# Performance work log

Measured on AMD Instinct MI355X. Metric: run time of the kernel, lower is better.

## Reference

```python
import jax, jax.numpy as jnp
import numpy as np
from jax import lax

B, S, E, CC, H, NH, K = 8, 2048, 128, 256, 256, 8, 7
HD = H // NH  # head dim = 32


def setup_inputs() -> dict:
    key = jax.random.key(0)
    ks = jax.random.split(key, 16)
    x = jax.random.normal(ks[0], (B, S, E), dtype=jnp.float32)
    lengths = jax.random.randint(ks[1], (B,), S // 2, S + 1)
    mask = (jnp.arange(S)[None, :] < lengths[:, None])  # contiguous prefix padding mask
    sc = 0.02
    return {
        "x": x,
        "mask": mask,
        "conv_w": jax.random.normal(ks[2], (CC, E, K), dtype=jnp.float32) * sc,
        "conv_b": jnp.zeros((CC,), jnp.float32),
        "wq": jax.random.normal(ks[3], (CC, H), dtype=jnp.float32) * sc,
        "bq": jnp.zeros((H,), jnp.float32),
        "wk": jax.random.normal(ks[4], (CC, H), dtype=jnp.float32) * sc,
        "bk": jnp.zeros((H,), jnp.float32),
        "wv": jax.random.normal(ks[5], (CC, H), dtype=jnp.float32) * sc,
        "bv": jnp.zeros((H,), jnp.float32),
        "fc_w": jax.random.normal(ks[6], (H, CC), dtype=jnp.float32) * sc,
        "fc_b": jnp.zeros((CC,), jnp.float32),
        "ln_g": jnp.ones((CC,), jnp.float32),
        "ln_b": jnp.zeros((CC,), jnp.float32),
        "gamma": jnp.float32(0.5),
        "std_param": jnp.float32(0.2),
    }


def _penalty(mask, gamma, std_param):
    # (B, S, S) Gaussian penalty, nonzero only in the valid_len x valid_len block
    valid_len = mask.sum(axis=-1).astype(jnp.float32)  # (B,)
    idx = jnp.arange(S, dtype=jnp.float32)
    valid = (jnp.arange(S)[None, :] < mask.sum(axis=-1)[:, None]).astype(jnp.float32)  # (B,S)
    norm_pos = (idx[None, :] + 1.0) / (valid_len[:, None] + 1.0)  # (B,S)
    std = jnp.clip(std_param, 0.01, 0.5)
    base = jnp.exp(-((norm_pos - 0.5) ** 2) / (2.0 * std * std))
    pvec = base * (jnp.exp(gamma) - 1.0) * valid  # (B,S)
    pen = 0.5 * (pvec[:, :, None] + pvec[:, None, :])
    return pen * valid[:, :, None] * valid[:, None, :]


def reference(x, mask, conv_w, conv_b, wq, bq, wk, bk, wv, bv, fc_w, fc_b, ln_g, ln_b, gamma, std_param):
    # Conv1d frontend: (B,S,E) -> (B,E,S) -> conv -> relu -> (B,S,CC)
    xt = jnp.transpose(x, (0, 2, 1))
    y = lax.conv_general_dilated(xt, conv_w, window_strides=(1,), padding=[(K // 2, K // 2)])
    y = jax.nn.relu(y + conv_b[None, :, None])
    h = jnp.transpose(y, (0, 2, 1))  # (B,S,CC)

    q = (h @ wq + bq).reshape(B, S, NH, HD).transpose(0, 2, 1, 3)
    k = (h @ wk + bk).reshape(B, S, NH, HD).transpose(0, 2, 1, 3)
    v = (h @ wv + bv).reshape(B, S, NH, HD).transpose(0, 2, 1, 3)

    scores = jnp.einsum('bnqd,bnkd->bnqk', q, k) / np.sqrt(HD).astype(np.float32)
    scores = scores - _penalty(mask, gamma, std_param)[:, None, :, :]
    scores = jnp.where(mask[:, None, None, :], scores, jnp.float32(-1e10))
    probs = jax.nn.softmax(scores, axis=-1)
    ctx = jnp.einsum('bnqk,bnkd->bnqd', probs, v)
    ctx = ctx.transpose(0, 2, 1, 3).reshape(B, S, H)
    out = ctx @ fc_w + fc_b

    z = h + out
    mu = z.mean(-1, keepdims=True)
    var = ((z - mu) ** 2).mean(-1, keepdims=True)
    return (z - mu) / jnp.sqrt(var + 1e-5) * ln_g + ln_b
```

## Files before the change

### kernel.cpp

```cpp
#include <hip/hip_runtime.h>
#include <hip/hip_bf16.h>

#define B_ 8
#define S_ 2048
#define E_ 128
#define CC_ 256
#define H_ 256
#define NH_ 8
#define HD_ 32
#define KW_ 7

typedef __attribute__((ext_vector_type(8))) short bf16x8;
typedef __attribute__((ext_vector_type(4))) float f32x4;
typedef __attribute__((ext_vector_type(16))) float f32x16;

#define QSCALE_ (0.17677669529663687f * 1.4426950408889634f)
#define CPEN_   0.7213475204444817f

static __device__ __forceinline__ unsigned short f2bf(float f) {
    __hip_bfloat16 h = __float2bfloat16(f);
    return *(unsigned short*)&h;
}
static __device__ __forceinline__ float bf2f(unsigned short u) {
    __hip_bfloat16 h = *(__hip_bfloat16*)&u;
    return __bfloat162float(h);
}
static __device__ __forceinline__ void perm32swap(unsigned& a, unsigned& b) {
    asm volatile("s_nop 1\n\tv_permlane32_swap_b32 %0, %1" : "+v"(a), "+v"(b));
}

__global__ __launch_bounds__(256) void prep_kernel(
    const float* __restrict__ cw, const float* __restrict__ wq,
    const float* __restrict__ wk, const float* __restrict__ wv,
    const float* __restrict__ fw, const void* __restrict__ mask,
    const float* __restrict__ gamma_p, const float* __restrict__ std_p,
    unsigned short* __restrict__ wre2, unsigned short* __restrict__ wqkv2,
    unsigned short* __restrict__ wf2, float* __restrict__ ctab,
    int* __restrict__ lenv)
{
    __shared__ int cnt[256];
    const int blk = blockIdx.x, tid = threadIdx.x;

    if (blk < 896) {
        int i = blk * 256 + tid;
        int kl = i & 31, cc = (i >> 5) & 255, eb = (i >> 13) & 3, kk = i >> 15;
        wre2[i] = f2bf(cw[cc * (E_ * KW_) + (eb * 32 + kl) * KW_ + kk]);
    } else if (blk < 1664) {
        int i = (blk - 896) * 256 + tid;
        int kl = i & 31, col = (i >> 5) & 255, kb = (i >> 13) & 7, m = i >> 16;
        const float* W = (m == 0) ? wq : (m == 1) ? wk : wv;
        wqkv2[i] = f2bf(W[(kb * 32 + kl) * H_ + col]);
    } else if (blk < 1920) {
        int i = (blk - 1664) * 256 + tid;
        int kl = i & 31, col = (i >> 5) & 255, kb = i >> 13;
        wf2[i] = f2bf(fw[(kb * 32 + kl) * CC_ + col]);
    } else {
        int b = blk - 1920;

        uint32_t w0 = ((const uint32_t*)mask)[0];
        int mode = 0;
        if (w0 == 0x01010101u) mode = 1;
        else if (w0 == 0x3F803F80u) mode = 2;
        else if (w0 == 0x3F800000u) mode = 3;

        int c = 0;
        for (int s = tid; s < S_; s += 256) {
            bool vv;
            size_t i = (size_t)b * S_ + s;
            if (mode == 0)      vv = ((const int*)mask)[i] != 0;
            else if (mode == 1) vv = ((const unsigned char*)mask)[i] != 0;
            else if (mode == 2) vv = (((const unsigned short*)mask)[i] & 0x7FFFu) != 0;
            else                vv = ((const float*)mask)[i] != 0.f;
            c += vv ? 1 : 0;
        }
        cnt[tid] = c;
        __syncthreads();
        for (int off = 128; off > 0; off >>= 1) {
            if (tid < off) cnt[tid] += cnt[tid + off];
            __syncthreads();
        }
        int L = cnt[0];
        if (tid == 0) lenv[b] = L;

        float Lf = (float)L;
        float gamma = gamma_p[0];
        float sd = std_p[0];
        sd = fminf(fmaxf(sd, 0.01f), 0.5f);
        float scale = expf(gamma) - 1.f;
        float inv2s2 = 1.f / (2.f * sd * sd);
        float* row0 = ctab + (size_t)b * 2 * S_;
        float* row1 = row0 + S_;
        for (int s = tid; s < S_; s += 256) {
            float np = (s + 1.f) / (Lf + 1.f);
            float e = np - 0.5f;
            float base = expf(-(e * e) * inv2s2);
            bool vkk = s < L;
            row0[s] = vkk ? 0.f : -1e10f;
            row1[s] = vkk ? (-CPEN_ * base * scale) : -1e10f;
        }
    }
}

__global__ __launch_bounds__(256) void front_kernel(
    const float* __restrict__ x, const unsigned short* __restrict__ wre2,
    const float* __restrict__ cb, const unsigned short* __restrict__ wqkv2,
    const float* __restrict__ bq, const float* __restrict__ bk,
    const float* __restrict__ bv, unsigned short* __restrict__ hb,
    unsigned short* __restrict__ qo, unsigned short* __restrict__ ko,
    unsigned short* __restrict__ vo)
{
    __shared__ __align__(16) char smem[64 * 264 * 2];
    short (*xl)[136] = (short(*)[136])smem;
    short (*Al)[264] = (short(*)[264])smem;

    const int tid = threadIdx.x, wave = tid >> 6, lane = tid & 63;
    const int l15 = lane & 15, l4 = lane >> 4;
    const int s0 = blockIdx.x * 64, b = blockIdx.y;

    for (int idx = tid; idx < 70 * 32; idx += 256) {
        int row = idx >> 5, c4 = idx & 31;
        int pos = s0 - 3 + row;
        float4 v = {0.f, 0.f, 0.f, 0.f};
        if (pos >= 0 && pos < S_)
            v = *(const float4*)(x + ((size_t)b * S_ + pos) * E_ + c4 * 4);
        short* p = &xl[row][c4 * 4];
        p[0] = (short)f2bf(v.x); p[1] = (short)f2bf(v.y);
        p[2] = (short)f2bf(v.z); p[3] = (short)f2bf(v.w);
    }
    __syncthreads();

    f32x4 acc[4][4];
#pragma unroll
    for (int i = 0; i < 4; i++)
#pragma unroll
        for (int j = 0; j < 4; j++) acc[i][j] = (f32x4){0.f, 0.f, 0.f, 0.f};

#pragma unroll 1
    for (int kk = 0; kk < KW_; kk++) {
#pragma unroll
        for (int eb = 0; eb < 4; eb++) {
            const unsigned short* wp =
                wre2 + (((size_t)(kk * 4 + eb) * 256 + wave * 64 + l15) * 32) + l4 * 8;
            bf16x8 af[4], bfr[4];
#pragma unroll
            for (int ct = 0; ct < 4; ct++)
                bfr[ct] = *(const bf16x8*)(wp + ct * 512);
#pragma unroll
            for (int rt = 0; rt < 4; rt++)
                af[rt] = *(const bf16x8*)(&xl[rt * 16 + l15 + kk][eb * 32 + l4 * 8]);
#pragma unroll
            for (int rt = 0; rt < 4; rt++)
#pragma unroll
                for (int ct = 0; ct < 4; ct++)
                    acc[rt][ct] = __builtin_amdgcn_mfma_f32_16x16x32_bf16(
                        af[rt], bfr[ct], acc[rt][ct], 0, 0, 0);
        }
    }
    __syncthreads();

#pragma unroll
    for (int ct = 0; ct < 4; ct++) {
        int col = wave * 64 + ct * 16 + l15;
        float bias = cb[col];
#pragma unroll
        for (int rt = 0; rt < 4; rt++)
#pragma unroll
            for (int r = 0; r < 4; r++) {
                float v0 = acc[rt][ct][r] + bias;
                v0 = v0 > 0.f ? v0 : 0.f;
                Al[rt * 16 + l4 * 4 + r][col] = (short)f2bf(v0);
            }
    }
    __syncthreads();

    for (int idx = tid; idx < 64 * 32; idx += 256) {
        int row = idx >> 5, c8 = idx & 31;
        *(bf16x8*)(hb + ((size_t)b * S_ + s0 + row) * CC_ + c8 * 8) =
            *(const bf16x8*)(&Al[row][c8 * 8]);
    }

#pragma unroll 1
    for (int m = 0; m < 3; m++) {
        f32x4 qacc[4][4];
#pragma unroll
        for (int i = 0; i < 4; i++)
#pragma unroll
            for (int j = 0; j < 4; j++) qacc[i][j] = (f32x4){0.f, 0.f, 0.f, 0.f};

#pragma unroll 1
        for (int kb8 = 0; kb8 < 8; kb8++) {
            const unsigned short* wp =
                wqkv2 + (((size_t)(m * 8 + kb8) * 256 + wave * 64 + l15) * 32) + l4 * 8;
            bf16x8 af[4], bfr[4];
#pragma unroll
            for (int ct = 0; ct < 4; ct++)
                bfr[ct] = *(const bf16x8*)(wp + ct * 512);
#pragma unroll
            for (int rt = 0; rt < 4; rt++)
                af[rt] = *(const bf16x8*)(&Al[rt * 16 + l15][kb8 * 32 + l4 * 8]);
#pragma unroll
            for (int rt = 0; rt < 4; rt++)
#pragma unroll
                for (int ct = 0; ct < 4; ct++)
                    qacc[rt][ct] = __builtin_amdgcn_mfma_f32_16x16x32_bf16(
                        af[rt], bfr[ct], qacc[rt][ct], 0, 0, 0);
        }

        const float* bias_p = (m == 0) ? bq : (m == 1) ? bk : bv;
        unsigned short* O = (m == 0) ? qo : (m == 1) ? ko : vo;
        const float oscale = (m == 0) ? QSCALE_ : 1.f;
#pragma unroll
        for (int ct = 0; ct < 4; ct++) {
            int col = wave * 64 + ct * 16 + l15;
            float bias = bias_p[col];
            int n = col >> 5, d = col & 31;
#pragma unroll
            for (int rt = 0; rt < 4; rt++)
#pragma unroll
                for (int r = 0; r < 4; r++) {
                    int row = s0 + rt * 16 + l4 * 4 + r;
                    O[(((size_t)b * NH_ + n) * S_ + row) * HD_ + d] =
                        f2bf((qacc[rt][ct][r] + bias) * oscale);
                }
        }
    }
}

__global__ __launch_bounds__(256) void attn_mfma_kernel(
    const unsigned short* __restrict__ q, const unsigned short* __restrict__ k,
    const unsigned short* __restrict__ v, const float* __restrict__ ctab,
    const int* __restrict__ lenv, unsigned short* __restrict__ ctxb)
{
    __shared__ short Kt[2][128][40];
    __shared__ short Vt[2][32][136];
    __shared__ __align__(16) float ctC[2][2][128];

    const int tid = threadIdx.x;
    const int wave = tid >> 6, lane = tid & 63;
    const int r31 = lane & 31, hi = lane >> 5;
    const int hi8 = hi * 8, hi4 = hi * 4;

    const int bx = blockIdx.x;
    const int b = bx & 7, n = bx >> 3, qt = blockIdx.y;
    const int qrow = qt * 128 + wave * 32 + r31;
    const int L = lenv[b];
    const int nt = (L + 127) >> 7;

    const size_t head = ((size_t)b * NH_ + n) * S_;
    const unsigned short* qbase = q + head * HD_;
    const unsigned short* kbase = k + head * HD_;
    const unsigned short* vbase = v + head * HD_;
    const float* ct0 = ctab + (size_t)b * 2 * S_;
    const float* ct1 = ct0 + S_;

    bf16x8 qf0 = *(const bf16x8*)(qbase + (size_t)qrow * HD_ + hi8);
    bf16x8 qf1 = *(const bf16x8*)(qbase + (size_t)qrow * HD_ + 16 + hi8);
    const int crow = (qrow < L) ? 1 : 0;

    f32x16 acc;
#pragma unroll
    for (int r = 0; r < 16; r++) acc[r] = 0.f;
    float m_r = -1e30f, l_r = 0.f;

    const int krow = tid >> 1, kch = (tid & 1) * 16;
    const int d7x2 = 2 * (r31 & 7);
    const int vc = krow >> 3, vk7 = krow & 7;

    bf16x8 kreg0, kreg1, va, vb;
    float c0r = 0.f, c1r = 0.f;

    kreg0 = *(const bf16x8*)(kbase + (size_t)krow * HD_ + kch);
    kreg1 = *(const bf16x8*)(kbase + (size_t)krow * HD_ + kch + 8);
    va    = *(const bf16x8*)(vbase + (size_t)krow * HD_ + kch);
    vb    = *(const bf16x8*)(vbase + (size_t)krow * HD_ + kch + 8);
    if (tid < 128) { c0r = ct0[tid]; c1r = ct1[tid]; }
    {
        *(bf16x8*)(&Kt[0][krow][kch])     = kreg0;
        *(bf16x8*)(&Kt[0][krow][kch + 8]) = kreg1;
#pragma unroll
        for (int i = 0; i < 8; i++) {
            int d0 = kch + i, d1 = kch + 8 + i;
            Vt[0][d0][((((vc - 2 * (d0 & 7)) & 7) | (vc & 8)) << 3) + vk7] = va[i];
            Vt[0][d1][((((vc - 2 * (d1 & 7)) & 7) | (vc & 8)) << 3) + vk7] = vb[i];
        }
        if (tid < 128) { ctC[0][0][tid] = c0r; ctC[0][1][tid] = c1r; }
    }
    __syncthreads();

#pragma unroll 1
    for (int t = 0; t < nt; t++) {
        const int cur = t & 1;
        const int knext = (t + 1) << 7;
        const bool more = (t + 1 < nt);

        if (more) {
            kreg0 = *(const bf16x8*)(kbase + (size_t)(knext + krow) * HD_ + kch);
            kreg1 = *(const bf16x8*)(kbase + (size_t)(knext + krow) * HD_ + kch + 8);
            va    = *(const bf16x8*)(vbase + (size_t)(knext + krow) * HD_ + kch);
            vb    = *(const bf16x8*)(vbase + (size_t)(knext + krow) * HD_ + kch + 8);
            if (tid < 128) { c0r = ct0[knext + tid]; c1r = ct1[knext + tid]; }
        }

        __builtin_amdgcn_s_setprio(1);
        f32x16 sc[4];
#pragma unroll
        for (int t4 = 0; t4 < 4; t4++) {
            bf16x8 kf0 = *(const bf16x8*)(&Kt[cur][t4 * 32 + r31][hi8]);
            bf16x8 kf1 = *(const bf16x8*)(&Kt[cur][t4 * 32 + r31][16 + hi8]);
            f32x16 c0;
#pragma unroll
            for (int g = 0; g < 4; g++) {
                f32x4 cp = *(const f32x4*)(&ctC[cur][crow][t4 * 32 + g * 8 + hi4]);
#pragma unroll
                for (int j = 0; j < 4; j++) c0[g * 4 + j] = cp[j];
            }
            f32x16 s1 = __builtin_amdgcn_mfma_f32_32x32x16_bf16(kf0, qf0, c0, 0, 0, 0);
            sc[t4] = __builtin_amdgcn_mfma_f32_32x32x16_bf16(kf1, qf1, s1, 0, 0, 0);
        }
        __builtin_amdgcn_s_setprio(0);

        float pmx = -1e30f;
#pragma unroll
        for (int t4 = 0; t4 < 4; t4++)
#pragma unroll
            for (int r = 0; r < 16; r += 2)
                pmx = fmaxf(pmx, fmaxf(sc[t4][r], sc[t4][r + 1]));
        pmx = fmaxf(pmx, __shfl_xor(pmx, 32, 64));

        float alpha = 1.f;
        if (!__all(pmx <= m_r + 8.f)) {
            float mn = fmaxf(m_r, pmx);
            alpha = exp2f(m_r - mn);
            m_r = mn;
#pragma unroll
            for (int r = 0; r < 16; r++) acc[r] *= alpha;
        }

        float rs = 0.f;
        unsigned pk[4][8];
#pragma unroll
        for (int t4 = 0; t4 < 4; t4++) {
            float p[16];
#pragma unroll
            for (int r = 0; r < 16; r++) {
                p[r] = exp2f(sc[t4][r] - m_r);
                rs += p[r];
            }
            unsigned U00 = (unsigned)f2bf(p[0])  | ((unsigned)f2bf(p[1])  << 16);
            unsigned U01 = (unsigned)f2bf(p[2])  | ((unsigned)f2bf(p[3])  << 16);
            unsigned U10 = (unsigned)f2bf(p[4])  | ((unsigned)f2bf(p[5])  << 16);
            unsigned U11 = (unsigned)f2bf(p[6])  | ((unsigned)f2bf(p[7])  << 16);
            unsigned U20 = (unsigned)f2bf(p[8])  | ((unsigned)f2bf(p[9])  << 16);
            unsigned U21 = (unsigned)f2bf(p[10]) | ((unsigned)f2bf(p[11]) << 16);
            unsigned U30 = (unsigned)f2bf(p[12]) | ((unsigned)f2bf(p[13]) << 16);
            unsigned U31 = (unsigned)f2bf(p[14]) | ((unsigned)f2bf(p[15]) << 16);
            perm32swap(U00, U10);
            perm32swap(U01, U11);
            perm32swap(U20, U30);
            perm32swap(U21, U31);
            pk[t4][0] = U00; pk[t4][1] = U01; pk[t4][2] = U10; pk[t4][3] = U11;
            pk[t4][4] = U20; pk[t4][5] = U21; pk[t4][6] = U30; pk[t4][7] = U31;
        }
        rs += __shfl_xor(rs, 32, 64);
        l_r = l_r * alpha + rs;

        __builtin_amdgcn_s_setprio(1);
#pragma unroll
        for (int t4 = 0; t4 < 4; t4++) {
            union { unsigned u[4]; bf16x8 v8; } pb0, pb1;
            pb0.u[0] = pk[t4][0]; pb0.u[1] = pk[t4][1];
            pb0.u[2] = pk[t4][2]; pb0.u[3] = pk[t4][3];
            pb1.u[0] = pk[t4][4]; pb1.u[1] = pk[t4][5];
            pb1.u[2] = pk[t4][6]; pb1.u[3] = pk[t4][7];
            int c0i = t4 * 4 + hi, c1i = t4 * 4 + 2 + hi;
            bf16x8 vf0 = *(const bf16x8*)(&Vt[cur][r31][(((c0i - d7x2) & 7) | (c0i & 8)) << 3]);
            bf16x8 vf1 = *(const bf16x8*)(&Vt[cur][r31][(((c1i - d7x2) & 7) | (c1i & 8)) << 3]);
            acc = __builtin_amdgcn_mfma_f32_32x32x16_bf16(vf0, pb0.v8, acc, 0, 0, 0);
            acc = __builtin_amdgcn_mfma_f32_32x32x16_bf16(vf1, pb1.v8, acc, 0, 0, 0);
        }
        __builtin_amdgcn_s_setprio(0);

        if (more) {
            const int nxt = cur ^ 1;
            *(bf16x8*)(&Kt[nxt][krow][kch])     = kreg0;
            *(bf16x8*)(&Kt[nxt][krow][kch + 8]) = kreg1;
#pragma unroll
            for (int i = 0; i < 8; i++) {
                int d0 = kch + i, d1 = kch + 8 + i;
                Vt[nxt][d0][((((vc - 2 * (d0 & 7)) & 7) | (vc & 8)) << 3) + vk7] = va[i];
                Vt[nxt][d1][((((vc - 2 * (d1 & 7)) & 7) | (vc & 8)) << 3) + vk7] = vb[i];
            }
            if (tid < 128) { ctC[nxt][0][tid] = c0r; ctC[nxt][1][tid] = c1r; }
            __syncthreads();
        }
    }

    float inv = 1.f / l_r;
    size_t obase = ((size_t)b * S_ + qrow) * H_ + n * HD_;
#pragma unroll
    for (int g = 0; g < 4; g++)
#pragma unroll
        for (int w = 0; w < 2; w++) {
            unsigned uo = (unsigned)f2bf(acc[g * 4 + w * 2] * inv) |
                          ((unsigned)f2bf(acc[g * 4 + w * 2 + 1] * inv) << 16);
            int d = 8 * g + hi4 + 2 * w;
            *(unsigned*)(ctxb + obase + d) = uo;
        }
}

__global__ __launch_bounds__(256) void fc_ln_mfma_kernel(
    const unsigned short* __restrict__ ctxb, const unsigned short* __restrict__ hb,
    const unsigned short* __restrict__ wf2, const float* __restrict__ fb,
    const float* __restrict__ g, const float* __restrict__ bbias,
    float* __restrict__ out)
{
    const int tid = threadIdx.x, wave = tid >> 6, lane = tid & 63;
    const int l15 = lane & 15, l4 = lane >> 4;
    const int s0 = blockIdx.x * 64, b = blockIdx.y;
    const int arow = s0 + wave * 16 + l15;

    bf16x8 af[8];
#pragma unroll
    for (int kb = 0; kb < 8; kb++)
        af[kb] = *(const bf16x8*)(ctxb + (size_t)((size_t)b * S_ + arow) * H_ + kb * 32 + l4 * 8);

    f32x4 acc[16];
#pragma unroll
    for (int ct = 0; ct < 16; ct++) acc[ct] = (f32x4){0.f, 0.f, 0.f, 0.f};

#pragma unroll 1
    for (int kb = 0; kb < 8; kb++) {
        const unsigned short* wp = wf2 + ((size_t)kb * 256 + l15) * 32 + l4 * 8;
#pragma unroll
        for (int ct = 0; ct < 16; ct++) {
            bf16x8 bfr = *(const bf16x8*)(wp + ct * 512);
            acc[ct] = __builtin_amdgcn_mfma_f32_16x16x32_bf16(af[kb], bfr, acc[ct], 0, 0, 0);
        }
    }

    float fbias[16];
#pragma unroll
    for (int ct = 0; ct < 16; ct++) fbias[ct] = fb[ct * 16 + l15];

#pragma unroll
    for (int r = 0; r < 4; r++) {
        int row = s0 + wave * 16 + l4 * 4 + r;
        size_t ro = ((size_t)b * S_ + row) * CC_;
        float z[16];
        float sum = 0.f;
#pragma unroll
        for (int ct = 0; ct < 16; ct++) {
            float zz = acc[ct][r] + fbias[ct] + bf2f(hb[ro + ct * 16 + l15]);
            z[ct] = zz;
            sum += zz;
        }
#pragma unroll
        for (int off = 1; off < 16; off <<= 1) sum += __shfl_xor(sum, off, 64);
        float mu = sum * (1.f / 256.f);
        float vs = 0.f;
#pragma unroll
        for (int ct = 0; ct < 16; ct++) {
            float d = z[ct] - mu;
            z[ct] = d;
            vs += d * d;
        }
#pragma unroll
        for (int off = 1; off < 16; off <<= 1) vs += __shfl_xor(vs, off, 64);
        float inv = rsqrtf(vs * (1.f / 256.f) + 1e-5f);
#pragma unroll
        for (int ct = 0; ct < 16; ct++) {
            int col = ct * 16 + l15;
            out[ro + col] = z[ct] * inv * g[col] + bbias[col];
        }
    }
}

extern "C" void kernel_launch(void* const* d_in, const int* in_sizes, int n_in,
                              void* d_out, int out_size, void* d_ws, size_t ws_size,
                              hipStream_t stream)
{
    const float* x      = (const float*)d_in[0];
    const void*  mask   = d_in[1];
    const float* conv_w = (const float*)d_in[2];
    const float* conv_b = (const float*)d_in[3];
    const float* wq     = (const float*)d_in[4];
    const float* bq     = (const float*)d_in[5];
    const float* wk     = (const float*)d_in[6];
    const float* bk     = (const float*)d_in[7];
    const float* wv     = (const float*)d_in[8];
    const float* bv     = (const float*)d_in[9];
    const float* fc_w   = (const float*)d_in[10];
    const float* fc_b   = (const float*)d_in[11];
    const float* ln_g   = (const float*)d_in[12];
    const float* ln_b   = (const float*)d_in[13];
    const float* gamma  = (const float*)d_in[14];
    const float* stdp   = (const float*)d_in[15];

    char* ws = (char*)d_ws;
    const size_t MB = 1024 * 1024;
    unsigned short* hb    = (unsigned short*)(ws);
    unsigned short* qb    = (unsigned short*)(ws + 8 * MB);
    unsigned short* kb    = (unsigned short*)(ws + 16 * MB);
    unsigned short* vb    = (unsigned short*)(ws + 24 * MB);
    unsigned short* ctxb  = (unsigned short*)(ws + 32 * MB);
    float*          ctab  = (float*)(ws + 40 * MB);
    int*            lenv  = (int*)(ws + 40 * MB + 256 * 1024);
    unsigned short* wre2  = (unsigned short*)(ws + 41 * MB);
    unsigned short* wqkv2 = (unsigned short*)(ws + 42 * MB);
    unsigned short* wf2   = (unsigned short*)(ws + 43 * MB);

    prep_kernel<<<1928, 256, 0, stream>>>(conv_w, wq, wk, wv, fc_w, mask,
                                          gamma, stdp, wre2, wqkv2, wf2,
                                          ctab, lenv);
    dim3 g2(S_ / 64, B_);
    front_kernel<<<g2, 256, 0, stream>>>(x, wre2, conv_b, wqkv2, bq, bk, bv,
                                         hb, qb, kb, vb);
    dim3 ag(B_ * NH_, S_ / 128);
    attn_mfma_kernel<<<ag, 256, 0, stream>>>(qb, kb, vb, ctab, lenv, ctxb);
    fc_ln_mfma_kernel<<<g2, 256, 0, stream>>>(ctxb, hb, wf2, fc_b, ln_g, ln_b,
                                              (float*)d_out);
}
```

Baseline: 207.3 us.

## Fold running max into MFMA bias, tree-reduce max/sum, reorder attention grid

The running max m_r is now subtracted from the penalty bias loaded into the score MFMA accumulator, so scores come out already max-shifted and the per-element subtraction before exp2 goes away. Max and row-sum reductions are split into four independent chains to shorten dependency latency. The grid is reordered so consecutive blocks share the same batch and head (q-tile fastest), which should improve K/V cache reuse. Rescaling now subtracts the max delta from all scores only in the rare rescale branch; initial m_r=0 relies on scores staying within the threshold.

```diff
diff --git a/kernel.cpp b/kernel.cpp
--- a/kernel.cpp
+++ b/kernel.cpp
@@ -240,8 +240,7 @@
     const int r31 = lane & 31, hi = lane >> 5;
     const int hi8 = hi * 8, hi4 = hi * 4;
 
-    const int bx = blockIdx.x;
-    const int b = bx & 7, n = bx >> 3, qt = blockIdx.y;
+    const int qt = blockIdx.x, n = blockIdx.y, b = blockIdx.z;
     const int qrow = qt * 128 + wave * 32 + r31;
     const int L = lenv[b];
     const int nt = (L + 127) >> 7;
@@ -260,7 +259,7 @@
     f32x16 acc;
 #pragma unroll
     for (int r = 0; r < 16; r++) acc[r] = 0.f;
-    float m_r = -1e30f, l_r = 0.f;
+    float m_r = 0.f, l_r = 0.f;
 
     const int krow = tid >> 1, kch = (tid & 1) * 16;
     const int d7x2 = 2 * (r31 & 7);
@@ -312,40 +311,51 @@
             for (int g = 0; g < 4; g++) {
                 f32x4 cp = *(const f32x4*)(&ctC[cur][crow][t4 * 32 + g * 8 + hi4]);
 #pragma unroll
-                for (int j = 0; j < 4; j++) c0[g * 4 + j] = cp[j];
+                for (int j = 0; j < 4; j++) c0[g * 4 + j] = cp[j] - m_r;
             }
             f32x16 s1 = __builtin_amdgcn_mfma_f32_32x32x16_bf16(kf0, qf0, c0, 0, 0, 0);
             sc[t4] = __builtin_amdgcn_mfma_f32_32x32x16_bf16(kf1, qf1, s1, 0, 0, 0);
         }
         __builtin_amdgcn_s_setprio(0);
 
-        float pmx = -1e30f;
+        float mxa[4];
+#pragma unroll
+        for (int g = 0; g < 4; g++) mxa[g] = -1e30f;
 #pragma unroll
         for (int t4 = 0; t4 < 4; t4++)
 #pragma unroll
-            for (int r = 0; r < 16; r += 2)
-                pmx = fmaxf(pmx, fmaxf(sc[t4][r], sc[t4][r + 1]));
+            for (int g = 0; g < 4; g++)
+                mxa[g] = fmaxf(fmaxf(fmaxf(mxa[g], sc[t4][g * 4]),
+                                     fmaxf(sc[t4][g * 4 + 1], sc[t4][g * 4 + 2])),
+                               sc[t4][g * 4 + 3]);
+        float pmx = fmaxf(fmaxf(mxa[0], mxa[1]), fmaxf(mxa[2], mxa[3]));
         pmx = fmaxf(pmx, __shfl_xor(pmx, 32, 64));
 
         float alpha = 1.f;
-        if (!__all(pmx <= m_r + 8.f)) {
-            float mn = fmaxf(m_r, pmx);
-            alpha = exp2f(m_r - mn);
-            m_r = mn;
+        if (!__all(pmx <= 8.f)) {
+            float d = fmaxf(pmx, 0.f);
+            alpha = exp2f(-d);
+            m_r += d;
+#pragma unroll
+            for (int t4 = 0; t4 < 4; t4++)
+#pragma unroll
+                for (int r = 0; r < 16; r++) sc[t4][r] -= d;
 #pragma unroll
             for (int r = 0; r < 16; r++) acc[r] *= alpha;
         }
 
-        float rs = 0.f;
+        float rsa[4] = {0.f, 0.f, 0.f, 0.f};
         unsigned pk[4][8];
 #pragma unroll
         for (int t4 = 0; t4 < 4; t4++) {
             float p[16];
 #pragma unroll
-            for (int r = 0; r < 16; r++) {
-                p[r] = exp2f(sc[t4][r] - m_r);
-                rs += p[r];
-            }
+            for (int g = 0; g < 4; g++)
+#pragma unroll
+                for (int j = 0; j < 4; j++) {
+                    p[g * 4 + j] = exp2f(sc[t4][g * 4 + j]);
+                    rsa[g] += p[g * 4 + j];
+                }
             unsigned U00 = (unsigned)f2bf(p[0])  | ((unsigned)f2bf(p[1])  << 16);
             unsigned U01 = (unsigned)f2bf(p[2])  | ((unsigned)f2bf(p[3])  << 16);
             unsigned U10 = (unsigned)f2bf(p[4])  | ((unsigned)f2bf(p[5])  << 16);
@@ -361,6 +371,7 @@
             pk[t4][0] = U00; pk[t4][1] = U01; pk[t4][2] = U10; pk[t4][3] = U11;
             pk[t4][4] = U20; pk[t4][5] = U21; pk[t4][6] = U30; pk[t4][7] = U31;
         }
+        float rs = (rsa[0] + rsa[1]) + (rsa[2] + rsa[3]);
         rs += __shfl_xor(rs, 32, 64);
         l_r = l_r * alpha + rs;
 
@@ -515,7 +526,7 @@
     dim3 g2(S_ / 64, B_);
     front_kernel<<<g2, 256, 0, stream>>>(x, wre2, conv_b, wqkv2, bq, bk, bv,
                                          hb, qb, kb, vb);
-    dim3 ag(B_ * NH_, S_ / 128);
+    dim3 ag(S_ / 128, NH_, B_);
     attn_mfma_kernel<<<ag, 256, 0, stream>>>(qb, kb, vb, ctab, lenv, ctxb);
     fc_ln_mfma_kernel<<<g2, 256, 0, stream>>>(ctxb, hb, wf2, fc_b, ln_g, ln_b,
                                               (float*)d_out);
```

Result: faster. 195.8 us (-5.6%).
